# Performance work log

Hardware: AMD Instinct MI355X
Metric: run time of the kernel (lower is better)

## Reference

```python
import jax, jax.numpy as jnp
import numpy as np

HEADS = 2
K_HOP = 2
RATIO = 0.8
NEG_SLOPE = 0.01


def seg_softmax(logits, seg, num_seg):
    # torch_geometric.utils.softmax: numerically stable segment softmax
    m = jax.ops.segment_max(logits, seg, num_segments=num_seg)
    e = jnp.exp(logits - m[seg])
    d = jax.ops.segment_sum(e, seg, num_segments=num_seg)
    return e / d[seg]


def _attention(key_value, query, seg, num_seg, Wk, W1, W2, W3):
    # Attention.forward with enable_BN=False; weights stored [in,out] so x@W == torch Linear
    a = key_value @ Wk
    h = jnp.concatenate([a, query, a - query, a * query], axis=-1)  # [N,4H]
    h = jax.nn.leaky_relu(h @ W1, NEG_SLOPE)
    h = jax.nn.leaky_relu(h @ W2, NEG_SLOPE)
    h = jax.nn.leaky_relu(h @ W3, NEG_SLOPE)  # [N,1]
    return seg_softmax(h[:, 0], seg, num_seg)[:, None]  # att_weights [N,1]


def setup_inputs():
    key = jax.random.key(0)
    ks = jax.random.split(key, 10)
    B, n, H, epg = 64, 64, 128, 2048
    N = B * n
    x = jax.random.normal(ks[0], (N, H), jnp.float32)
    src = jax.random.randint(ks[1], (B, epg), 0, n)
    dst = jax.random.randint(ks[2], (B, epg), 0, n)
    off = (jnp.arange(B) * n)[:, None]
    edge_index = jnp.stack([(src + off).reshape(-1), (dst + off).reshape(-1)], 0)
    edge_weight = jax.random.uniform(ks[3], (B * epg,), jnp.float32)
    target_x = jax.random.normal(ks[4], (B, H), jnp.float32)
    batch_ixs = jnp.repeat(jnp.arange(B), n)
    s = lambda i, sh: jax.random.normal(ks[i], sh, jnp.float32) / np.sqrt(sh[-2])
    # index 0=cluster_att, 1=query_att, 2=cluster_att2, 3=query_att2
    att_Wk = s(5, (4, H, H))
    att_W1 = s(6, (4, 4 * H, 2 * H))
    att_W2 = s(7, (4, 2 * H, H))
    att_W3 = s(8, (4, H, 1))
    lin_W = s(9, (HEADS, H, H))
    return dict(x=x, edge_index=edge_index, edge_weight=edge_weight, target_x=target_x,
                batch_ixs=batch_ixs, att_Wk=att_Wk, att_W1=att_W1, att_W2=att_W2,
                att_W3=att_W3, lin_W=lin_W)


def reference(x, edge_index, edge_weight, target_x, batch_ixs, att_Wk, att_W1, att_W2, att_W3, lin_W):
    N, H = x.shape
    B = target_x.shape[0]
    n = N // B
    # ---- gcn_norm with self loops (fill 1.0) ----
    loop = jnp.arange(N)
    row = jnp.concatenate([edge_index[0], loop])
    col = jnp.concatenate([edge_index[1], loop])
    w = jnp.concatenate([edge_weight, jnp.ones((N,), edge_weight.dtype)])
    deg = jax.ops.segment_sum(w, col, num_segments=N)
    dinv = jnp.where(deg > 0, jax.lax.rsqrt(jnp.maximum(deg, 1e-12)), 0.0)
    ew = dinv[row] * w * dinv[col]  # [L]
    # ---- k-hop propagation ----
    def hop(v):
        return jax.ops.segment_sum(v[row] * ew[:, None], col, num_segments=N)
    x_q = x
    for _ in range(K_HOP):
        x_q = hop(x_q)
    qt = target_x[batch_ixs]  # repeat_interleave by per-graph counts (sorted batch)
    # ---- multi-head edge attention (reuse_att_w=True, dropout=0 -> E identical per head) ----
    f1 = _attention(x, x_q, batch_ixs, B, att_Wk[0], att_W1[0], att_W2[0], att_W3[0])
    f2 = _attention(x, qt, batch_ixs, B, att_Wk[1], att_W1[1], att_W2[1], att_W3[1])
    E = jax.nn.leaky_relu(f1[col] + f2[row], NEG_SLOPE)  # [L,1]
    E = seg_softmax(E[:, 0], col, N)[:, None]
    x_c = jnp.zeros_like(x)
    E_g = jnp.zeros((row.shape[0], 1), x.dtype)
    agg = jax.ops.segment_sum(x[row] * E, col, num_segments=N)
    for h in range(HEADS):
        x_c = x_c + jax.nn.leaky_relu(x + agg @ lin_W[h], NEG_SLOPE)
        E_g = E_g + E
    x_c = x_c / HEADS
    E_g = E_g / HEADS
    # ---- second k-hop + cluster scoring ----
    x_q2 = x_c
    for _ in range(K_HOP):
        x_q2 = hop(x_q2)
    g1 = _attention(x_c, x_q2, batch_ixs, B, att_Wk[2], att_W1[2], att_W2[2], att_W3[2])
    g2 = _attention(x_c, qt, batch_ixs, B, att_Wk[3], att_W1[3], att_W2[3], att_W3[3])
    # stack over heads then mean == g1+g2 (same attention modules reused per head)
    cluster_score = seg_softmax((g1 + g2)[:, 0], batch_ixs, B)  # [N]
    # ---- per-graph topk (ratio) ----
    kk = int(np.ceil(RATIO * n))
    _, idx = jax.lax.top_k(cluster_score.reshape(B, n), kk)  # descending, matches PyG topk
    perm = (idx + (jnp.arange(B) * n)[:, None]).reshape(-1)  # [Nk]
    x_out = x[perm] * cluster_score[perm][:, None]
    batch_out = batch_ixs[perm]
    # ---- S^T A S (dense equivalent of SparseTensor triple product) ----
    A_d = jnp.zeros((N, N), x.dtype).at[row, col].add(ew)
    S_d = jnp.zeros((N, N), x.dtype).at[row, col].add(E_g[:, 0])
    S_p = S_d[:, perm]  # S[:, perm] -> [N, Nk]
    A2 = S_p.T @ (A_d @ S_p)  # [Nk, Nk]
    Nk = perm.shape[0]
    A2 = A2.at[jnp.arange(Nk), jnp.arange(Nk)].set(1.0)  # fill_diag(1.0)
    return x_out, A2, batch_out, perm
```

## Files before the change

### kernel.cpp

```cpp
#include <hip/hip_runtime.h>

#define KK 52
#define NKOUT 3328
#define NEG 0.01f

typedef __attribute__((ext_vector_type(8))) __bf16 bf16x8;
typedef __attribute__((ext_vector_type(16))) float floatx16;

__device__ __forceinline__ float lrelu(float v){ return v > 0.f ? v : NEG*v; }

#define SW(r, ko) ((r)*40 + ((ko) ^ ((((r)>>3)&3) << 3)))

__device__ __forceinline__ void split_store8(const float* vv, __bf16* P0, __bf16* P1, __bf16* P2, int addr){
  bf16x8 p1, p2, p3;
  #pragma unroll
  for (int j = 0; j < 8; j++){
    __bf16 b1 = (__bf16)vv[j];
    float r1 = vv[j] - (float)b1;
    __bf16 b2 = (__bf16)r1;
    float r2 = r1 - (float)b2;
    p1[j] = b1; p2[j] = b2; p3[j] = (__bf16)r2;
  }
  *(bf16x8*)(P0 + addr) = p1;
  *(bf16x8*)(P1 + addr) = p2;
  *(bf16x8*)(P2 + addr) = p3;
}

__device__ __forceinline__ void mfma6(const __bf16* A0, const __bf16* A1, const __bf16* A2,
                                      const __bf16* B0, const __bf16* B1, const __bf16* B2,
                                      int aoff, int boff, floatx16* acc){
  bf16x8 a1 = *(const bf16x8*)(A0 + aoff);
  bf16x8 a2 = *(const bf16x8*)(A1 + aoff);
  bf16x8 a3 = *(const bf16x8*)(A2 + aoff);
  bf16x8 b1 = *(const bf16x8*)(B0 + boff);
  bf16x8 b2 = *(const bf16x8*)(B1 + boff);
  bf16x8 b3 = *(const bf16x8*)(B2 + boff);
  floatx16 c = *acc;
  c = __builtin_amdgcn_mfma_f32_32x32x16_bf16(a1,b1,c,0,0,0);
  c = __builtin_amdgcn_mfma_f32_32x32x16_bf16(a1,b2,c,0,0,0);
  c = __builtin_amdgcn_mfma_f32_32x32x16_bf16(a2,b1,c,0,0,0);
  c = __builtin_amdgcn_mfma_f32_32x32x16_bf16(a1,b3,c,0,0,0);
  c = __builtin_amdgcn_mfma_f32_32x32x16_bf16(a3,b1,c,0,0,0);
  c = __builtin_amdgcn_mfma_f32_32x32x16_bf16(a2,b2,c,0,0,0);
  *acc = c;
}

__device__ __forceinline__ void g_gemm(const float* A0, int ldA,
                                       const float* __restrict__ W0, int ldW, int K,
                                       __bf16* pb, floatx16* oA, floatx16* oB){
  __bf16 *As0 = pb, *As1 = pb+2560, *As2 = pb+5120;
  __bf16 *Bs0 = pb+7680, *Bs1 = pb+12800, *Bs2 = pb+17920;
  int tid = threadIdx.x;
  int sar = tid >> 2, sako = (tid & 3)*8;
  int bn = tid & 127, bk = (tid >> 7)*16;
  int wv_ = tid >> 6, L = tid & 63, m = L & 31, half = L >> 5;
  int rA = 32*(wv_ & 1) + m, rB0 = (wv_ >> 1)*32 + m, rB1 = rB0 + 64;
  const float* arow = A0 + (size_t)sar*ldA;
  floatx16 accA, accB;
  #pragma unroll
  for (int i = 0; i < 16; i++){ accA[i] = 0.f; accB[i] = 0.f; }
  float ra[8], wv[16];
  {
    float4 v0 = *(const float4*)(arow + sako);
    float4 v1 = *(const float4*)(arow + sako + 4);
    ra[0]=v0.x; ra[1]=v0.y; ra[2]=v0.z; ra[3]=v0.w; ra[4]=v1.x; ra[5]=v1.y; ra[6]=v1.z; ra[7]=v1.w;
    #pragma unroll
    for (int j = 0; j < 16; j++) wv[j] = W0[(size_t)(bk + j)*ldW + bn];
  }
  for (int k0 = 0; k0 < K; k0 += 32){
    split_store8(ra, As0, As1, As2, SW(sar, sako));
    split_store8(wv,     Bs0, Bs1, Bs2, SW(bn, bk));
    split_store8(wv + 8, Bs0, Bs1, Bs2, SW(bn, bk + 8));
    __syncthreads();
    int k1 = k0 + 32;
    float ra2[8], wv2[16];
    if (k1 < K){
      float4 v0 = *(const float4*)(arow + k1 + sako);
      float4 v1 = *(const float4*)(arow + k1 + sako + 4);
      ra2[0]=v0.x; ra2[1]=v0.y; ra2[2]=v0.z; ra2[3]=v0.w; ra2[4]=v1.x; ra2[5]=v1.y; ra2[6]=v1.z; ra2[7]=v1.w;
      #pragma unroll
      for (int j = 0; j < 16; j++) wv2[j] = W0[(size_t)(k1 + bk + j)*ldW + bn];
    }
    #pragma unroll
    for (int kg = 0; kg < 2; kg++){
      int ko = kg*16 + half*8;
      mfma6(As0,As1,As2, Bs0,Bs1,Bs2, SW(rA,ko), SW(rB0,ko), &accA);
      mfma6(As0,As1,As2, Bs0,Bs1,Bs2, SW(rA,ko), SW(rB1,ko), &accB);
    }
    __syncthreads();
    if (k1 < K){
      #pragma unroll
      for (int j = 0; j < 8; j++) ra[j] = ra2[j];
      #pragma unroll
      for (int j = 0; j < 16; j++) wv[j] = wv2[j];
    }
  }
  *oA = accA; *oB = accB;
}

__device__ __forceinline__ void g_gemm64(const float* __restrict__ A0, int ldA,
                                         const float* __restrict__ W0, int ldW, int K,
                                         __bf16* pb, floatx16* oC){
  __bf16 *As0 = pb, *As1 = pb+2560, *As2 = pb+5120;
  __bf16 *Bs0 = pb+7680, *Bs1 = pb+10240, *Bs2 = pb+12800;
  int tid = threadIdx.x;
  int sar = tid >> 2, sako = (tid & 3)*8;
  int bn = tid & 63, bk = (tid >> 6)*8;
  int wv_ = tid >> 6, L = tid & 63, m = L & 31, half = L >> 5;
  int rA = 32*(wv_ & 1) + m, rB = 32*(wv_ >> 1) + m;
  const float* arow = A0 + (size_t)sar*ldA;
  floatx16 acc;
  #pragma unroll
  for (int i = 0; i < 16; i++) acc[i] = 0.f;
  float ra[8], wv[8];
  {
    float4 v0 = *(const float4*)(arow + sako);
    float4 v1 = *(const float4*)(arow + sako + 4);
    ra[0]=v0.x; ra[1]=v0.y; ra[2]=v0.z; ra[3]=v0.w; ra[4]=v1.x; ra[5]=v1.y; ra[6]=v1.z; ra[7]=v1.w;
    #pragma unroll
    for (int j = 0; j < 8; j++) wv[j] = W0[(size_t)(bk + j)*ldW + bn];
  }
  for (int k0 = 0; k0 < K; k0 += 32){
    split_store8(ra, As0, As1, As2, SW(sar, sako));
    split_store8(wv, Bs0, Bs1, Bs2, SW(bn, bk));
    __syncthreads();
    int k1 = k0 + 32;
    float ra2[8], wv2[8];
    if (k1 < K){
      float4 v0 = *(const float4*)(arow + k1 + sako);
      float4 v1 = *(const float4*)(arow + k1 + sako + 4);
      ra2[0]=v0.x; ra2[1]=v0.y; ra2[2]=v0.z; ra2[3]=v0.w; ra2[4]=v1.x; ra2[5]=v1.y; ra2[6]=v1.z; ra2[7]=v1.w;
      #pragma unroll
      for (int j = 0; j < 8; j++) wv2[j] = W0[(size_t)(k1 + bk + j)*ldW + bn];
    }
    #pragma unroll
    for (int kg = 0; kg < 2; kg++){
      int ko = kg*16 + half*8;
      mfma6(As0,As1,As2, Bs0,Bs1,Bs2, SW(rA,ko), SW(rB,ko), &acc);
    }
    __syncthreads();
    if (k1 < K){
      #pragma unroll
      for (int j = 0; j < 8; j++){ ra[j] = ra2[j]; wv[j] = wv2[j]; }
    }
  }
  *oC = acc;
}

__device__ __forceinline__ void g_gemm_h64(const float* __restrict__ arow, const float* __restrict__ qrow,
                                           const float* __restrict__ W1fz, int colbase,
                                           __bf16* pb, floatx16* oC){
  __bf16 *As0 = pb, *As1 = pb+2560, *As2 = pb+5120;
  __bf16 *Bs0 = pb+7680, *Bs1 = pb+10240, *Bs2 = pb+12800;
  int tid = threadIdx.x;
  int sar = tid >> 2, sako = (tid & 3)*8;
  int bn = tid & 63, bk = (tid >> 6)*8;
  int col = colbase + bn;
  int wv_ = tid >> 6, L = tid & 63, m = L & 31, half = L >> 5;
  int rA = 32*(wv_ & 1) + m, rB = 32*(wv_ >> 1) + m;
  auto loadA = [&](int k0, float* r){
    int seg = k0 >> 7, kl = (k0 & 127) + sako;
    if (seg == 0){
      float4 a0 = *(const float4*)(arow + kl), a1 = *(const float4*)(arow + kl + 4);
      r[0]=a0.x; r[1]=a0.y; r[2]=a0.z; r[3]=a0.w; r[4]=a1.x; r[5]=a1.y; r[6]=a1.z; r[7]=a1.w;
    } else if (seg == 1){
      float4 q0 = *(const float4*)(qrow + kl), q1 = *(const float4*)(qrow + kl + 4);
      r[0]=q0.x; r[1]=q0.y; r[2]=q0.z; r[3]=q0.w; r[4]=q1.x; r[5]=q1.y; r[6]=q1.z; r[7]=q1.w;
    } else {
      float4 a0 = *(const float4*)(arow + kl), a1 = *(const float4*)(arow + kl + 4);
      float4 q0 = *(const float4*)(qrow + kl), q1 = *(const float4*)(qrow + kl + 4);
      r[0]=a0.x*q0.x; r[1]=a0.y*q0.y; r[2]=a0.z*q0.z; r[3]=a0.w*q0.w;
      r[4]=a1.x*q1.x; r[5]=a1.y*q1.y; r[6]=a1.z*q1.z; r[7]=a1.w*q1.w;
    }
  };
  auto loadB = [&](int k0, float* r){
    #pragma unroll
    for (int j = 0; j < 8; j++) r[j] = W1fz[(size_t)(k0 + bk + j)*256 + col];
  };
  floatx16 acc;
  #pragma unroll
  for (int i = 0; i < 16; i++) acc[i] = 0.f;
  float ra[8], wv[8];
  loadA(0, ra); loadB(0, wv);
  for (int k0 = 0; k0 < 384; k0 += 32){
    split_store8(ra, As0, As1, As2, SW(sar, sako));
    split_store8(wv, Bs0, Bs1, Bs2, SW(bn, bk));
    __syncthreads();
    int k1 = k0 + 32;
    float ra2[8], wv2[8];
    if (k1 < 384){ loadA(k1, ra2); loadB(k1, wv2); }
    #pragma unroll
    for (int kg = 0; kg < 2; kg++){
      int ko = kg*16 + half*8;
      mfma6(As0,As1,As2, Bs0,Bs1,Bs2, SW(rA,ko), SW(rB,ko), &acc);
    }
    __syncthreads();
    if (k1 < 384){
      #pragma unroll
      for (int j = 0; j < 8; j++){ ra[j] = ra2[j]; wv[j] = wv2[j]; }
    }
  }
  *oC = acc;
}

__device__ __forceinline__ void c_write(floatx16 accA, floatx16 accB, float* C0, int ldC, int act){
  int tid = threadIdx.x, wv_ = tid >> 6, L = tid & 63, m = L & 31, half = L >> 5;
  int rB0 = (wv_ >> 1)*32 + m, rB1 = rB0 + 64;
  int row0 = 32*(wv_ & 1) + 4*half;
  #pragma unroll
  for (int reg = 0; reg < 16; reg++){
    int row = row0 + (reg & 3) + 8*(reg >> 2);
    float va = accA[reg], vb = accB[reg];
    if (act){ va = lrelu(va); vb = lrelu(vb); }
    C0[(size_t)row*ldC + rB0] = va;
    C0[(size_t)row*ldC + rB1] = vb;
  }
}

__device__ __forceinline__ void c_write64(floatx16 acc, float* C0, int ldC, int act){
  int tid = threadIdx.x, wv_ = tid >> 6, L = tid & 63, m = L & 31, half = L >> 5;
  int col = 32*(wv_ >> 1) + m;
  int row0 = 32*(wv_ & 1) + 4*half;
  #pragma unroll
  for (int reg = 0; reg < 16; reg++){
    int row = row0 + (reg & 3) + 8*(reg >> 2);
    float v = acc[reg];
    if (act) v = lrelu(v);
    C0[(size_t)row*ldC + col] = v;
  }
}

__device__ __forceinline__ void hop2_run(const float* A, const float* VfullL,
                                         const float* srcG, float* dstG,
                                         float* Vt, float* Tt, int fbeg, int fend){
  int tid = threadIdx.x;
  int tc = (tid & 31)*2, tf = (tid >> 5)*4;
  for (int f0 = fbeg; f0 < fend; f0 += 32){
    if (!VfullL){
      for (int o = tid; o < 2048; o += 256){
        int r = o >> 5, f = o & 31;
        Vt[o] = srcG[r*128 + f0 + f];
      }
      __syncthreads();
    }
    float a00,a01,a02,a03,a10,a11,a12,a13;
    a00=a01=a02=a03=a10=a11=a12=a13=0.f;
    for (int r = 0; r < 64; r++){
      float x0 = A[r*64 + tc], x1 = A[r*64 + tc + 1];
      float4 v4 = VfullL ? *(const float4*)&VfullL[r*128 + f0 + tf]
                         : *(const float4*)&Vt[r*32 + tf];
      a00 += x0*v4.x; a01 += x0*v4.y; a02 += x0*v4.z; a03 += x0*v4.w;
      a10 += x1*v4.x; a11 += x1*v4.y; a12 += x1*v4.z; a13 += x1*v4.w;
    }
    *(float4*)&Tt[tc*32 + tf]     = make_float4(a00,a01,a02,a03);
    *(float4*)&Tt[(tc+1)*32 + tf] = make_float4(a10,a11,a12,a13);
    __syncthreads();
    a00=a01=a02=a03=a10=a11=a12=a13=0.f;
    for (int r = 0; r < 64; r++){
      float x0 = A[r*64 + tc], x1 = A[r*64 + tc + 1];
      float4 v4 = *(const float4*)&Tt[r*32 + tf];
      a00 += x0*v4.x; a01 += x0*v4.y; a02 += x0*v4.z; a03 += x0*v4.w;
      a10 += x1*v4.x; a11 += x1*v4.y; a12 += x1*v4.z; a13 += x1*v4.w;
    }
    *(float4*)(dstG + tc*128 + f0 + tf)     = make_float4(a00,a01,a02,a03);
    *(float4*)(dstG + (tc+1)*128 + f0 + tf) = make_float4(a10,a11,a12,a13);
    __syncthreads();
  }
}

__global__ __launch_bounds__(256) void k_p0(const int* __restrict__ ei, const float* __restrict__ ew,
                                            const float* __restrict__ x, const float* __restrict__ Wk,
                                            const float* __restrict__ W1,
                                            float* A_g, float* M_g, float* xq, float* a_buf, float* W1f,
                                            float* outA2){
  __shared__ __align__(16) char POOL[57856];
  float* pf = (float*)POOL;
  __bf16* pb = (__bf16*)POOL;
  int blk = blockIdx.x, tid = threadIdx.x;
  if (blk < 128){
    int b = blk >> 1, fh = blk & 1;
    float* Ws = pf; float* Mc = pf + 4096; float* dv = pf + 8192;
    for (int i = tid; i < 4096; i += 256){ Ws[i] = 0.f; Mc[i] = 0.f; }
    __syncthreads();
    const int* r0 = ei + b*2048;
    const int* c0 = ei + 64*2048 + b*2048;
    const float* w0 = ew + b*2048;
    int base = b*64;
    for (int e = tid; e < 2048; e += 256){
      int r = r0[e] - base, c = c0[e] - base;
      atomicAdd(&Ws[r*64 + c], w0[e]);
      atomicAdd(&Mc[r*64 + c], 1.f);
    }
    if (tid < 64){ atomicAdd(&Ws[tid*65], 1.f); atomicAdd(&Mc[tid*65], 1.f); }
    __syncthreads();
    if (tid < 64){
      float d = 0.f;
      for (int r = 0; r < 64; r++) d += Ws[r*64 + tid];
      dv[tid] = d > 0.f ? rsqrtf(fmaxf(d, 1e-12f)) : 0.f;
    }
    __syncthreads();
    for (int i = tid; i < 4096; i += 256){
      int r = i >> 6, c = i & 63;
      float a = dv[r]*Ws[i]*dv[c];
      Ws[i] = a;
      if (fh == 0){
        A_g[b*4096 + i] = a;
        M_g[b*4096 + i] = Mc[i];
      }
    }
    __syncthreads();
    hop2_run(Ws, nullptr, x + (size_t)b*8192, xq + (size_t)b*8192, pf + 8256, pf + 10304,
             fh*64, fh*64 + 64);
  } else if (blk < 256){
    int idx = blk - 128, z = idx >> 6, b = idx & 63;
    floatx16 cA, cB;
    g_gemm(x + (size_t)b*8192, 128, Wk + (size_t)z*16384, 128, 128, pb, &cA, &cB);
    c_write(cA, cB, a_buf + (size_t)z*524288 + (size_t)b*8192, 128, 0);
  } else if (blk < 320){
    int idx0 = (blk - 256)*6144;
    for (int i = tid; i < 6144; i += 256){
      int g = idx0 + i;
      int zz = g / 98304;
      int r = g - zz*98304;
      int kr = r >> 8, c = r & 255;
      const float* Wz = W1 + (size_t)zz*131072;
      float v;
      if (kr < 128)       v = Wz[kr*256 + c] + Wz[(kr + 256)*256 + c];
      else if (kr < 256)  v = Wz[kr*256 + c] - Wz[(kr + 128)*256 + c];
      else                v = Wz[(kr + 128)*256 + c];
      W1f[g] = v;
    }
  } else {
    float4* p = (float4*)outA2;
    int base = (blk - 320)*1024 + tid;
    #pragma unroll
    for (int i = 0; i < 4; i++) p[base + i*256] = make_float4(0.f,0.f,0.f,0.f);
  }
}

__global__ __launch_bounds__(256) void k_h1(const float* __restrict__ a_buf, const float* __restrict__ q0,
                                            const float* __restrict__ tgt, const float* __restrict__ W1fp,
                                            float* h1){
  __shared__ __align__(16) char POOL[30720];
  __bf16* pb = (__bf16*)POOL;
  int blk = blockIdx.x, tid = threadIdx.x;
  int b = blk >> 3, z = (blk >> 2) & 1, nq = blk & 3;
  int sar = tid >> 2;
  const float* arow = a_buf + (size_t)z*524288 + ((size_t)b*64 + sar)*128;
  const float* qrow = z ? (tgt + (size_t)b*128) : (q0 + ((size_t)b*64 + sar)*128);
  floatx16 c;
  g_gemm_h64(arow, qrow, W1fp + (size_t)z*98304, nq*64, pb, &c);
  c_write64(c, h1 + (size_t)z*1048576 + (size_t)b*16384 + nq*64, 256, 1);
}

__global__ __launch_bounds__(256) void k_w2p(const float* __restrict__ h1, const float* __restrict__ W2,
                                             const float* __restrict__ W3, float* __restrict__ lp){
  __shared__ __align__(16) char POOL[30720];
  __shared__ float lgp[128];
  __bf16* pb = (__bf16*)POOL;
  int blk = blockIdx.x, tid = threadIdx.x;
  int b = blk >> 2, z = (blk >> 1) & 1, nh = blk & 1;
  floatx16 c;
  g_gemm64(h1 + (size_t)z*1048576 + (size_t)b*16384, 256,
           W2 + (size_t)z*32768 + nh*64, 128, 256, pb, &c);
  int wv_ = tid >> 6, L = tid & 63, m = L & 31, half = L >> 5;
  int col = 32*(wv_ >> 1) + m;
  float w = W3[z*128 + nh*64 + col];
  float v[16];
  #pragma unroll
  for (int reg = 0; reg < 16; reg++) v[reg] = lrelu(c[reg])*w;
  #pragma unroll
  for (int off = 1; off < 32; off <<= 1)
    #pragma unroll
    for (int reg = 0; reg < 16; reg++) v[reg] += __shfl_xor(v[reg], off);
  if (m == 0){
    #pragma unroll
    for (int reg = 0; reg < 16; reg++) lgp[wv_*32 + half*16 + reg] = v[reg];
  }
  __syncthreads();
  if (tid < 64){
    int row = tid, rh = row >> 5, rem = row & 31;
    int hf = (rem >> 2) & 1, rg = (rem & 3) + 4*(rem >> 3);
    float p = lgp[rh*32 + hf*16 + rg] + lgp[(rh + 2)*32 + hf*16 + rg];
    lp[(z*2 + nh)*4096 + b*64 + row] = p;
  }
}

__global__ __launch_bounds__(256) void k_edgelin(const float* __restrict__ M_g, const float* __restrict__ lp,
                                                 const float* __restrict__ x, const float* __restrict__ linW,
                                                 const float* __restrict__ A_g,
                                                 float* S_g, float* xcb, float* xq2){
  __shared__ __align__(16) char POOL[128512];
  __bf16* pb = (__bf16*)POOL;
  float* f1s = (float*)(POOL + 46080);
  float* f2s = (float*)(POOL + 46336);
  float* Mc  = (float*)(POOL + 46592);
  float* xb  = (float*)(POOL + 62976);
  float* aggL= (float*)(POOL + 95744);
  int b = blockIdx.x, tid = threadIdx.x;
  for (int i = tid; i < 4096; i += 256) Mc[i] = M_g[b*4096 + i];
  for (int i = tid*4; i < 8192; i += 1024)
    *(float4*)&xb[i] = *(const float4*)(x + (size_t)b*8192 + i);
  if (tid < 128){
    int z = tid >> 6, r = tid & 63;
    float d = lp[(z*2)*4096 + b*64 + r] + lp[(z*2 + 1)*4096 + b*64 + r];
    float l = lrelu(d);
    float mx = l;
    #pragma unroll
    for (int off = 32; off; off >>= 1) mx = fmaxf(mx, __shfl_xor(mx, off));
    float e = expf(l - mx);
    float s = e;
    #pragma unroll
    for (int off = 32; off; off >>= 1) s += __shfl_xor(s, off);
    (z ? f2s : f1s)[r] = e/s;
  }
  __syncthreads();
  {
    int c = tid >> 2, sub = tid & 3;
    float m = -1e30f;
    for (int r = sub; r < 64; r += 4)
      if (Mc[r*64 + c] > 0.f) m = fmaxf(m, lrelu(f1s[c] + f2s[r]));
    m = fmaxf(m, __shfl_xor(m, 1));
    m = fmaxf(m, __shfl_xor(m, 2));
    float s = 0.f;
    for (int r = sub; r < 64; r += 4){
      float mc = Mc[r*64 + c];
      if (mc > 0.f) s += mc*expf(lrelu(f1s[c] + f2s[r]) - m);
    }
    s += __shfl_xor(s, 1);
    s += __shfl_xor(s, 2);
    for (int r = sub; r < 64; r += 4){
      float mc = Mc[r*64 + c];
      float v = 0.f;
      if (mc > 0.f) v = mc*expf(lrelu(f1s[c] + f2s[r]) - m)/s;
      Mc[r*64 + c] = v;
    }
  }
  __syncthreads();
  for (int i = tid; i < 4096; i += 256) S_g[b*4096 + i] = Mc[i];
  {
    int tc = (tid & 15)*4, tf = (tid >> 4)*8;
    float acc[4][8];
    #pragma unroll
    for (int i = 0; i < 4; i++)
      #pragma unroll
      for (int j = 0; j < 8; j++) acc[i][j] = 0.f;
    for (int r = 0; r < 64; r++){
      float4 e4 = *(const float4*)&Mc[r*64 + tc];
      float4 x0 = *(const float4*)&xb[r*128 + tf];
      float4 x1 = *(const float4*)&xb[r*128 + tf + 4];
      float e_[4] = {e4.x,e4.y,e4.z,e4.w};
      float x_[8] = {x0.x,x0.y,x0.z,x0.w,x1.x,x1.y,x1.z,x1.w};
      #pragma unroll
      for (int ci = 0; ci < 4; ci++)
        #pragma unroll
        for (int fj = 0; fj < 8; fj++) acc[ci][fj] += e_[ci]*x_[fj];
    }
    #pragma unroll
    for (int ci = 0; ci < 4; ci++){
      *(float4*)&aggL[(tc+ci)*128 + tf]     = make_float4(acc[ci][0],acc[ci][1],acc[ci][2],acc[ci][3]);
      *(float4*)&aggL[(tc+ci)*128 + tf + 4] = make_float4(acc[ci][4],acc[ci][5],acc[ci][6],acc[ci][7]);
    }
  }
  __syncthreads();
  floatx16 h0A, h0B, h1A, h1B2;
  g_gemm(aggL, 128, linW, 128, 128, pb, &h0A, &h0B);
  g_gemm(aggL, 128, linW + 16384, 128, 128, pb, &h1A, &h1B2);
  {
    int wv_ = tid >> 6, L = tid & 63, m = L & 31, half = L >> 5;
    int rB0 = (wv_ >> 1)*32 + m, rB1 = rB0 + 64, row0 = 32*(wv_ & 1) + 4*half;
    #pragma unroll
    for (int reg = 0; reg < 16; reg++){
      int row = row0 + (reg & 3) + 8*(reg >> 2);
      float xv0 = xb[row*128 + rB0];
      float v0 = 0.5f*(lrelu(xv0 + h0A[reg]) + lrelu(xv0 + h1A[reg]));
      xb[row*128 + rB0] = v0;
      xcb[(size_t)b*8192 + row*128 + rB0] = v0;
      float xv1 = xb[row*128 + rB1];
      float v1 = 0.5f*(lrelu(xv1 + h0B[reg]) + lrelu(xv1 + h1B2[reg]));
      xb[row*128 + rB1] = v1;
      xcb[(size_t)b*8192 + row*128 + rB1] = v1;
    }
  }
  float* Ab = (float*)POOL;
  float* Tt = (float*)(POOL + 16384);
  for (int i = tid*4; i < 4096; i += 1024)
    *(float4*)&Ab[i] = *(const float4*)(A_g + b*4096 + i);
  __syncthreads();
  hop2_run(Ab, xb, nullptr, xq2 + (size_t)b*8192, Tt, Tt, 0, 128);
}

__global__ __launch_bounds__(256) void k_wkg(const float* __restrict__ xcb, const float* __restrict__ Wkg,
                                             float* a_buf){
  __shared__ __align__(16) char POOL[30720];
  __bf16* pb = (__bf16*)POOL;
  int blk = blockIdx.x;
  int b = blk >> 2, z = (blk >> 1) & 1, nh = blk & 1;
  floatx16 c;
  g_gemm64(xcb + (size_t)b*8192, 128, Wkg + (size_t)z*16384 + nh*64, 128, 128, pb, &c);
  c_write64(c, a_buf + (size_t)z*524288 + (size_t)b*8192 + nh*64, 128, 0);
}

__global__ __launch_bounds__(256) void k_A2c(const float* __restrict__ lp, const float* __restrict__ x,
                                             const float* __restrict__ A_g, const float* __restrict__ S_g,
                                             float* outA2, float* outX, float* outB, float* outP){
  __shared__ __align__(16) float At[64*68];
  __shared__ __align__(16) float Sp[64*56];
  __shared__ __align__(16) float Tq[64*56];
  __shared__ int pi[64];
  __shared__ float pv[64];
  int b = blockIdx.x, tid = threadIdx.x;
  if (tid < 64){
    int lane = tid;
    float f[2];
    #pragma unroll
    for (int z = 0; z < 2; z++){
      float d = lp[(z*2)*4096 + b*64 + lane] + lp[(z*2 + 1)*4096 + b*64 + lane];
      float l = lrelu(d);
      float mx = l;
      #pragma unroll
      for (int off = 32; off; off >>= 1) mx = fmaxf(mx, __shfl_xor(mx, off));
      float e = expf(l - mx);
      float sm = e;
      #pragma unroll
      for (int off = 32; off; off >>= 1) sm += __shfl_xor(sm, off);
      f[z] = e/sm;
    }
    float l = f[0] + f[1];
    float m = l;
    #pragma unroll
    for (int off = 32; off; off >>= 1) m = fmaxf(m, __shfl_xor(m, off));
    float e = expf(l - m);
    float sm = e;
    #pragma unroll
    for (int off = 32; off; off >>= 1) sm += __shfl_xor(sm, off);
    float v = e/sm;
    int idx = lane;
    #pragma unroll
    for (int k = 2; k <= 64; k <<= 1){
      #pragma unroll
      for (int j = k >> 1; j > 0; j >>= 1){
        float ov = __shfl_xor(v, j);
        int   oi = __shfl_xor(idx, j);
        bool ascBlock = (lane & k) == 0;
        bool iAmLow   = (lane & j) == 0;
        bool otherPrec = (ov > v) || (ov == v && oi < idx);
        bool take = (ascBlock == iAmLow) ? otherPrec : !otherPrec;
        if (take){ v = ov; idx = oi; }
      }
    }
    pi[lane] = idx; pv[lane] = v;
    if (lane < KK){
      outB[b*KK + lane] = (float)b;
      outP[b*KK + lane] = (float)(b*64 + idx);
    }
  }
  __syncthreads();
  for (int o = tid*4; o < KK*128; o += 1024){
    int j = o >> 7, f = o & 127;
    float4 xv = *(const float4*)(x + ((size_t)b*64 + pi[j])*128 + f);
    float sv = pv[j];
    *(float4*)(outX + (size_t)b*KK*128 + o) = make_float4(xv.x*sv, xv.y*sv, xv.z*sv, xv.w*sv);
  }
  for (int idx = tid; idx < 4096; idx += 256){
    int i = idx >> 6, k = idx & 63;
    At[k*68 + i] = A_g[b*4096 + idx];
  }
  for (int idx = tid; idx < 4096; idx += 256){
    int k = idx >> 6, t = idx & 63;
    if (t < 56) Sp[k*56 + t] = (t < KK) ? S_g[b*4096 + k*64 + pi[t]] : 0.f;
  }
  __syncthreads();
  if (tid < 224){
    int i0 = (tid/14)*4, t0 = (tid % 14)*4;
    float acc[4][4];
    #pragma unroll
    for (int a = 0; a < 4; a++)
      #pragma unroll
      for (int c = 0; c < 4; c++) acc[a][c] = 0.f;
    for (int k = 0; k < 64; k++){
      float4 a4 = *(const float4*)&At[k*68 + i0];
      float4 s4 = *(const float4*)&Sp[k*56 + t0];
      float a_[4] = {a4.x,a4.y,a4.z,a4.w};
      float s_[4] = {s4.x,s4.y,s4.z,s4.w};
      #pragma unroll
      for (int ii = 0; ii < 4; ii++)
        #pragma unroll
        for (int tt = 0; tt < 4; tt++) acc[ii][tt] += a_[ii]*s_[tt];
    }
    #pragma unroll
    for (int ii = 0; ii < 4; ii++)
      *(float4*)&Tq[(i0+ii)*56 + t0] = make_float4(acc[ii][0],acc[ii][1],acc[ii][2],acc[ii][3]);
  }
  __syncthreads();
  if (tid < 169){
    int a0 = (tid/13)*4, t0 = (tid % 13)*4;
    float acc[4][4];
    #pragma unroll
    for (int a = 0; a < 4; a++)
      #pragma unroll
      for (int c = 0; c < 4; c++) acc[a][c] = 0.f;
    for (int i = 0; i < 64; i++){
      float4 s4 = *(const float4*)&Sp[i*56 + a0];
      float4 t4 = *(const float4*)&Tq[i*56 + t0];
      float s_[4] = {s4.x,s4.y,s4.z,s4.w};
      float t_[4] = {t4.x,t4.y,t4.z,t4.w};
      #pragma unroll
      for (int aa = 0; aa < 4; aa++)
        #pragma unroll
        for (int tt = 0; tt < 4; tt++) acc[aa][tt] += s_[aa]*t_[tt];
    }
    #pragma unroll
    for (int aa = 0; aa < 4; aa++){
      int a = a0 + aa;
      float4 o;
      o.x = (a == t0    ) ? 1.f : acc[aa][0];
      o.y = (a == t0 + 1) ? 1.f : acc[aa][1];
      o.z = (a == t0 + 2) ? 1.f : acc[aa][2];
      o.w = (a == t0 + 3) ? 1.f : acc[aa][3];
      *(float4*)(outA2 + (size_t)(b*KK + a)*NKOUT + b*KK + t0) = o;
    }
  }
}

extern "C" void kernel_launch(void* const* d_in, const int* in_sizes, int n_in,
                              void* d_out, int out_size, void* d_ws, size_t ws_size,
                              hipStream_t stream){
  const float* x    = (const float*)d_in[0];
  const int*   ei   = (const int*)d_in[1];
  const float* ew   = (const float*)d_in[2];
  const float* tgt  = (const float*)d_in[3];
  const float* Wk   = (const float*)d_in[5];
  const float* W1   = (const float*)d_in[6];
  const float* W2   = (const float*)d_in[7];
  const float* W3   = (const float*)d_in[8];
  const float* linW = (const float*)d_in[9];
  float* out = (float*)d_out;

  float* wf   = (float*)d_ws;
  float* A_g  = wf;
  float* M_g  = wf + 262144;
  float* S_g  = wf + 524288;
  float* xq   = wf + 786432;
  float* xq2  = wf + 1310720;
  float* xcb  = wf + 2359296;
  float* a_buf= wf + 2883584;
  float* h1   = wf + 3932160;
  float* lp   = wf + 6029312;
  float* W1f  = wf + 6045696;

  float* outX  = out;
  float* outA2 = out + 425984;
  float* outB  = out + 425984 + 11075584;
  float* outP  = outB + NKOUT;

  k_p0<<<dim3(3024), dim3(256), 0, stream>>>(ei, ew, x, Wk, W1, A_g, M_g, xq, a_buf, W1f, outA2);
  k_h1<<<dim3(512), dim3(256), 0, stream>>>(a_buf, xq, tgt, W1f, h1);
  k_w2p<<<dim3(256), dim3(256), 0, stream>>>(h1, W2, W3, lp);
  k_edgelin<<<dim3(64), dim3(256), 0, stream>>>(M_g, lp, x, linW, A_g, S_g, xcb, xq2);
  k_wkg<<<dim3(256), dim3(256), 0, stream>>>(xcb, Wk + 2*16384, a_buf);
  k_h1<<<dim3(512), dim3(256), 0, stream>>>(a_buf, xq2, tgt, W1f + 2*98304, h1);
  k_w2p<<<dim3(256), dim3(256), 0, stream>>>(h1, W2 + 2*32768, W3 + 2*128, lp);
  k_A2c<<<dim3(64), dim3(256), 0, stream>>>(lp, x, A_g, S_g, outA2, outX, outB, outP);
}
```

Before: 227.8 us.

## Precompute x@linW in first kernel and split edge-hop kernel across feature halves

Uses associativity to reorder (E^T x) @ linW as E^T (x @ linW). The two x@linW products are computed by extra blocks of the first, input-only kernel, so they run in parallel with other setup work. The edge kernel then only does the E^T aggregation on precomputed projections. That removes the bf16-split GEMMs and lets the kernel run as 128 blocks, each handling one feature half, instead of 64 blocks. The cost is extra workspace traffic for the xl0/xl1 buffers, and the Mc/edge-weight setup is now recomputed redundantly in both half-blocks.

```diff
diff --git a/kernel.cpp b/kernel.cpp
--- a/kernel.cpp
+++ b/kernel.cpp
@@ -230,8 +230,8 @@
   }
 }
 
-__device__ __forceinline__ void hop2_run(const float* A, const float* VfullL,
-                                         const float* srcG, float* dstG,
+__device__ __forceinline__ void hop2_run(const float* A, const float* VfullL, int ldV,
+                                         const float* srcG, float* dstG, int dstOff,
                                          float* Vt, float* Tt, int fbeg, int fend){
   int tid = threadIdx.x;
   int tc = (tid & 31)*2, tf = (tid >> 5)*4;
@@ -247,7 +247,7 @@
     a00=a01=a02=a03=a10=a11=a12=a13=0.f;
     for (int r = 0; r < 64; r++){
       float x0 = A[r*64 + tc], x1 = A[r*64 + tc + 1];
-      float4 v4 = VfullL ? *(const float4*)&VfullL[r*128 + f0 + tf]
+      float4 v4 = VfullL ? *(const float4*)&VfullL[r*ldV + f0 + tf]
                          : *(const float4*)&Vt[r*32 + tf];
       a00 += x0*v4.x; a01 += x0*v4.y; a02 += x0*v4.z; a03 += x0*v4.w;
       a10 += x1*v4.x; a11 += x1*v4.y; a12 += x1*v4.z; a13 += x1*v4.w;
@@ -262,17 +262,17 @@
       a00 += x0*v4.x; a01 += x0*v4.y; a02 += x0*v4.z; a03 += x0*v4.w;
       a10 += x1*v4.x; a11 += x1*v4.y; a12 += x1*v4.z; a13 += x1*v4.w;
     }
-    *(float4*)(dstG + tc*128 + f0 + tf)     = make_float4(a00,a01,a02,a03);
-    *(float4*)(dstG + (tc+1)*128 + f0 + tf) = make_float4(a10,a11,a12,a13);
+    *(float4*)(dstG + tc*128 + dstOff + f0 + tf)     = make_float4(a00,a01,a02,a03);
+    *(float4*)(dstG + (tc+1)*128 + dstOff + f0 + tf) = make_float4(a10,a11,a12,a13);
     __syncthreads();
   }
 }
 
 __global__ __launch_bounds__(256) void k_p0(const int* __restrict__ ei, const float* __restrict__ ew,
                                             const float* __restrict__ x, const float* __restrict__ Wk,
-                                            const float* __restrict__ W1,
+                                            const float* __restrict__ W1, const float* __restrict__ linW,
                                             float* A_g, float* M_g, float* xq, float* a_buf, float* W1f,
-                                            float* outA2){
+                                            float* xl0, float* xl1, float* outA2){
   __shared__ __align__(16) char POOL[57856];
   float* pf = (float*)POOL;
   __bf16* pb = (__bf16*)POOL;
@@ -309,7 +309,7 @@
       }
     }
     __syncthreads();
-    hop2_run(Ws, nullptr, x + (size_t)b*8192, xq + (size_t)b*8192, pf + 8256, pf + 10304,
+    hop2_run(Ws, nullptr, 0, x + (size_t)b*8192, xq + (size_t)b*8192, 0, pf + 8256, pf + 10304,
              fh*64, fh*64 + 64);
   } else if (blk < 256){
     int idx = blk - 128, z = idx >> 6, b = idx & 63;
@@ -330,11 +330,16 @@
       else                v = Wz[(kr + 128)*256 + c];
       W1f[g] = v;
     }
-  } else {
+  } else if (blk < 3024){
     float4* p = (float4*)outA2;
     int base = (blk - 320)*1024 + tid;
     #pragma unroll
     for (int i = 0; i < 4; i++) p[base + i*256] = make_float4(0.f,0.f,0.f,0.f);
+  } else {
+    int idx = blk - 3024, z = idx >> 6, b = idx & 63;
+    floatx16 cA, cB;
+    g_gemm(x + (size_t)b*8192, 128, linW + (size_t)z*16384, 128, 128, pb, &cA, &cB);
+    c_write(cA, cB, (z ? xl1 : xl0) + (size_t)b*8192, 128, 0);
   }
 }
 
@@ -386,21 +391,26 @@
   }
 }
 
-__global__ __launch_bounds__(256) void k_edgelin(const float* __restrict__ M_g, const float* __restrict__ lp,
-                                                 const float* __restrict__ x, const float* __restrict__ linW,
-                                                 const float* __restrict__ A_g,
+__global__ __launch_bounds__(256) void k_edgehop(const float* __restrict__ M_g, const float* __restrict__ lp,
+                                                 const float* __restrict__ x, const float* __restrict__ xl0g,
+                                                 const float* __restrict__ xl1g, const float* __restrict__ A_g,
                                                  float* S_g, float* xcb, float* xq2){
-  __shared__ __align__(16) char POOL[128512];
-  __bf16* pb = (__bf16*)POOL;
-  float* f1s = (float*)(POOL + 46080);
-  float* f2s = (float*)(POOL + 46336);
-  float* Mc  = (float*)(POOL + 46592);
-  float* xb  = (float*)(POOL + 62976);
-  float* aggL= (float*)(POOL + 95744);
-  int b = blockIdx.x, tid = threadIdx.x;
+  __shared__ __align__(16) float Mc[4096];
+  __shared__ __align__(16) float xh[4096];
+  __shared__ __align__(16) float xl0h[4096];
+  __shared__ __align__(16) float xl1h[4096];
+  __shared__ __align__(16) float Ab[4096];
+  __shared__ __align__(16) float Tt[2048];
+  __shared__ float f1s[64], f2s[64];
+  int blk = blockIdx.x, b = blk >> 1, fh = blk & 1, tid = threadIdx.x;
+  int foff = fh*64;
   for (int i = tid; i < 4096; i += 256) Mc[i] = M_g[b*4096 + i];
-  for (int i = tid*4; i < 8192; i += 1024)
-    *(float4*)&xb[i] = *(const float4*)(x + (size_t)b*8192 + i);
+  for (int o = tid*4; o < 4096; o += 1024){
+    int r = o >> 6, f = o & 63;
+    *(float4*)&xh[o]   = *(const float4*)(x    + (size_t)b*8192 + r*128 + foff + f);
+    *(float4*)&xl0h[o] = *(const float4*)(xl0g + (size_t)b*8192 + r*128 + foff + f);
+    *(float4*)&xl1h[o] = *(const float4*)(xl1g + (size_t)b*8192 + r*128 + foff + f);
+  }
   if (tid < 128){
     int z = tid >> 6, r = tid & 63;
     float d = lp[(z*2)*4096 + b*64 + r] + lp[(z*2 + 1)*4096 + b*64 + r];
@@ -437,57 +447,48 @@
     }
   }
   __syncthreads();
-  for (int i = tid; i < 4096; i += 256) S_g[b*4096 + i] = Mc[i];
+  if (fh == 0)
+    for (int i = tid; i < 4096; i += 256) S_g[b*4096 + i] = Mc[i];
   {
-    int tc = (tid & 15)*4, tf = (tid >> 4)*8;
-    float acc[4][8];
+    int tc = (tid & 15)*4, tf = (tid >> 4)*4;
+    float a0[4][4], a1[4][4];
     #pragma unroll
     for (int i = 0; i < 4; i++)
       #pragma unroll
-      for (int j = 0; j < 8; j++) acc[i][j] = 0.f;
+      for (int j = 0; j < 4; j++){ a0[i][j] = 0.f; a1[i][j] = 0.f; }
     for (int r = 0; r < 64; r++){
       float4 e4 = *(const float4*)&Mc[r*64 + tc];
-      float4 x0 = *(const float4*)&xb[r*128 + tf];
-      float4 x1 = *(const float4*)&xb[r*128 + tf + 4];
+      float4 p0 = *(const float4*)&xl0h[r*64 + tf];
+      float4 p1 = *(const float4*)&xl1h[r*64 + tf];
       float e_[4] = {e4.x,e4.y,e4.z,e4.w};
-      float x_[8] = {x0.x,x0.y,x0.z,x0.w,x1.x,x1.y,x1.z,x1.w};
+      float p0_[4] = {p0.x,p0.y,p0.z,p0.w};
+      float p1_[4] = {p1.x,p1.y,p1.z,p1.w};
       #pragma unroll
       for (int ci = 0; ci < 4; ci++)
         #pragma unroll
-        for (int fj = 0; fj < 8; fj++) acc[ci][fj] += e_[ci]*x_[fj];
-    }
+        for (int fj = 0; fj < 4; fj++){
+          a0[ci][fj] += e_[ci]*p0_[fj];
+          a1[ci][fj] += e_[ci]*p1_[fj];
+        }
+    }
+    __syncthreads();
     #pragma unroll
     for (int ci = 0; ci < 4; ci++){
-      *(float4*)&aggL[(tc+ci)*128 + tf]     = make_float4(acc[ci][0],acc[ci][1],acc[ci][2],acc[ci][3]);
-      *(float4*)&aggL[(tc+ci)*128 + tf + 4] = make_float4(acc[ci][4],acc[ci][5],acc[ci][6],acc[ci][7]);
-    }
-  }
-  __syncthreads();
-  floatx16 h0A, h0B, h1A, h1B2;
-  g_gemm(aggL, 128, linW, 128, 128, pb, &h0A, &h0B);
-  g_gemm(aggL, 128, linW + 16384, 128, 128, pb, &h1A, &h1B2);
-  {
-    int wv_ = tid >> 6, L = tid & 63, m = L & 31, half = L >> 5;
-    int rB0 = (wv_ >> 1)*32 + m, rB1 = rB0 + 64, row0 = 32*(wv_ & 1) + 4*half;
-    #pragma unroll
-    for (int reg = 0; reg < 16; reg++){
-      int row = row0 + (reg & 3) + 8*(reg >> 2);
-      float xv0 = xb[row*128 + rB0];
-      float v0 = 0.5f*(lrelu(xv0 + h0A[reg]) + lrelu(xv0 + h1A[reg]));
-      xb[row*128 + rB0] = v0;
-      xcb[(size_t)b*8192 + row*128 + rB0] = v0;
-      float xv1 = xb[row*128 + rB1];
-      float v1 = 0.5f*(lrelu(xv1 + h0B[reg]) + lrelu(xv1 + h1B2[reg]));
-      xb[row*128 + rB1] = v1;
-      xcb[(size_t)b*8192 + row*128 + rB1] = v1;
-    }
-  }
-  float* Ab = (float*)POOL;
-  float* Tt = (float*)(POOL + 16384);
+      int c = tc + ci;
+      float4 xv = *(const float4*)&xh[c*64 + tf];
+      float4 o;
+      o.x = 0.5f*(lrelu(xv.x + a0[ci][0]) + lrelu(xv.x + a1[ci][0]));
+      o.y = 0.5f*(lrelu(xv.y + a0[ci][1]) + lrelu(xv.y + a1[ci][1]));
+      o.z = 0.5f*(lrelu(xv.z + a0[ci][2]) + lrelu(xv.z + a1[ci][2]));
+      o.w = 0.5f*(lrelu(xv.w + a0[ci][3]) + lrelu(xv.w + a1[ci][3]));
+      *(float4*)&xh[c*64 + tf] = o;
+      *(float4*)(xcb + (size_t)b*8192 + c*128 + foff + tf) = o;
+    }
+  }
   for (int i = tid*4; i < 4096; i += 1024)
     *(float4*)&Ab[i] = *(const float4*)(A_g + b*4096 + i);
   __syncthreads();
-  hop2_run(Ab, xb, nullptr, xq2 + (size_t)b*8192, Tt, Tt, 0, 128);
+  hop2_run(Ab, xh, 64, nullptr, xq2 + (size_t)b*8192, foff, Tt, Tt, 0, 64);
 }
 
 __global__ __launch_bounds__(256) void k_wkg(const float* __restrict__ xcb, const float* __restrict__ Wkg,
@@ -643,21 +644,24 @@
   float* S_g  = wf + 524288;
   float* xq   = wf + 786432;
   float* xq2  = wf + 1310720;
+  float* xl0  = wf + 1835008;
   float* xcb  = wf + 2359296;
   float* a_buf= wf + 2883584;
   float* h1   = wf + 3932160;
   float* lp   = wf + 6029312;
   float* W1f  = wf + 6045696;
+  float* xl1  = wf + 6438912;
 
   float* outX  = out;
   float* outA2 = out + 425984;
   float* outB  = out + 425984 + 11075584;
   float* outP  = outB + NKOUT;
 
-  k_p0<<<dim3(3024), dim3(256), 0, stream>>>(ei, ew, x, Wk, W1, A_g, M_g, xq, a_buf, W1f, outA2);
+  k_p0<<<dim3(3152), dim3(256), 0, stream>>>(ei, ew, x, Wk, W1, linW, A_g, M_g, xq, a_buf, W1f,
+                                             xl0, xl1, outA2);
   k_h1<<<dim3(512), dim3(256), 0, stream>>>(a_buf, xq, tgt, W1f, h1);
   k_w2p<<<dim3(256), dim3(256), 0, stream>>>(h1, W2, W3, lp);
-  k_edgelin<<<dim3(64), dim3(256), 0, stream>>>(M_g, lp, x, linW, A_g, S_g, xcb, xq2);
+  k_edgehop<<<dim3(128), dim3(256), 0, stream>>>(M_g, lp, x, xl0, xl1, A_g, S_g, xcb, xq2);
   k_wkg<<<dim3(256), dim3(256), 0, stream>>>(xcb, Wk + 2*16384, a_buf);
   k_h1<<<dim3(512), dim3(256), 0, stream>>>(a_buf, xq2, tgt, W1f + 2*98304, h1);
   k_w2p<<<dim3(256), dim3(256), 0, stream>>>(h1, W2 + 2*32768, W3 + 2*128, lp);
```

New measurement: 210.5 us. 7.6% less time.
